# Performance work log

Measured on AMD Instinct MI355X. Metric: run time of the kernel, lower is better.

The kernel has to match this reference:

```python
import jax, jax.numpy as jnp
import numpy as np


def _gumbel_from_uniform(u):
    # u in (0,1) -> standard Gumbel noise
    u = jnp.clip(u, 1e-6, 1.0 - 1e-6)
    return -jnp.log(-jnp.log(u))


def _lsq(x, s, num_bits):
    # LSQ fake-quant: scale, clamp to signed range, round (STE), rescale.
    Qp = 2 ** (num_bits - 1) - 1
    Qn = -(2 ** (num_bits - 1))
    xs = x / s
    xc = jnp.clip(xs, Qn, Qp)
    xr = xc + jax.lax.stop_gradient(jnp.round(xc) - xc)
    return xr * s


def _hard_gumbel_softmax(logits, g, tau):
    y = jax.nn.softmax((logits + g) / tau, axis=-1)
    hard = jax.nn.one_hot(jnp.argmax(y, axis=-1), y.shape[-1], dtype=y.dtype)
    return hard + y - jax.lax.stop_gradient(y)


def setup_inputs() -> dict:
    key = jax.random.key(0)
    ks = jax.random.split(key, 16)
    B, L, K, N = 32, 1024, 64, 8
    v = jax.random.normal(ks[0], (B, L, K, 2), dtype=jnp.float32)
    H = jax.random.normal(ks[1], (B, L, N, K, 2), dtype=jnp.float32)
    local_snr = jax.random.uniform(ks[2], (B, L, K, 1), dtype=jnp.float32)
    g_demod = _gumbel_from_uniform(jax.random.uniform(ks[3], (B, L, K, 3), dtype=jnp.float32))
    g_channel = _gumbel_from_uniform(jax.random.uniform(ks[4], (B, L, K, 3), dtype=jnp.float32))
    # policy MLP params (in,out layout), kaiming-ish init
    W1 = jax.random.normal(ks[5], (5, 32), dtype=jnp.float32) * (2.0 / 5) ** 0.5
    b1 = jnp.zeros((32,), dtype=jnp.float32)
    W2 = jax.random.normal(ks[6], (32, 32), dtype=jnp.float32) * (2.0 / 32) ** 0.5
    b2 = jnp.zeros((32,), dtype=jnp.float32)
    Wd = jax.random.normal(ks[7], (32, 3), dtype=jnp.float32) * (1.0 / 32) ** 0.5
    bd = jnp.zeros((3,), dtype=jnp.float32)
    Wc = jax.random.normal(ks[8], (32, 3), dtype=jnp.float32) * (1.0 / 32) ** 0.5
    bc = jnp.zeros((3,), dtype=jnp.float32)
    # LSQ step sizes (scalars) matching init_s of the torch module
    s2d = jnp.float32(0.5)
    s4d = jnp.float32(0.1)
    s2c = jnp.float32(0.5)
    s4c = jnp.float32(0.1)
    return dict(v=v, H=H, local_snr=local_snr, g_demod=g_demod, g_channel=g_channel,
                W1=W1, b1=b1, W2=W2, b2=b2, Wd=Wd, bd=bd, Wc=Wc, bc=bc,
                s2d=s2d, s4d=s4d, s2c=s2c, s4c=s4c)


def reference(v, H, local_snr, g_demod, g_channel,
              W1, b1, W2, b2, Wd, bd, Wc, bc, s2d, s4d, s2c, s4c):
    tau = 1.0
    B, L, K, _ = v.shape
    N = H.shape[2]
    # channel power features: sum over antennas and re/im -> (B,L,K)
    h_power = jnp.sum(H * H, axis=(2, 4))
    channel_norm = h_power[..., None]                      # (B,L,K,1)
    avg_power = jnp.broadcast_to(jnp.mean(h_power, axis=1, keepdims=True), (B, L, K))[..., None]
    pin = jnp.concatenate([v[..., 0:1], v[..., 1:2], local_snr, channel_norm, avg_power], axis=-1)  # (B,L,K,5)
    # tiny router MLP
    h = jax.nn.relu(pin @ W1 + b1)
    h = jax.nn.relu(h @ W2 + b2)
    logits_demod = h @ Wd + bd                              # (B,L,K,3)
    logits_channel = h @ Wc + bc
    w_demod = _hard_gumbel_softmax(logits_demod, g_demod, tau)
    w_channel = _hard_gumbel_softmax(logits_channel, g_channel, tau)
    # weighted combine of fake-quantized branches (0-bit branch contributes 0)
    v_q = w_demod[..., 1:2] * _lsq(v, s2d, 2) + w_demod[..., 2:3] * _lsq(v, s4d, 4)
    w_ch = w_channel[:, :, None]                            # (B,L,1,K,3) broadcast over antennas
    H_q = w_ch[..., 1:2] * _lsq(H, s2c, 2) + w_ch[..., 2:3] * _lsq(H, s4c, 4)
    expected_bits_demod = w_demod[..., 1] * 4.0 + w_demod[..., 2] * 8.0
    expected_bits_channel = w_channel[..., 1] * (2.0 * N * 2) + w_channel[..., 2] * (2.0 * N * 4)
    return (v_q, H_q, expected_bits_demod, expected_bits_channel, w_demod, w_channel)
```

## Files before the change

kernel.cpp:

```cpp
#include <hip/hip_runtime.h>

namespace {
constexpr int Bb = 32, Ll = 1024, Kk = 64, Nn = 8;
constexpr int BLK = Bb * Ll * Kk;
constexpr long long HFLOATS = (long long)BLK * Nn * 2;
constexpr int CH = 16;
constexpr int LCH = Ll / CH;

constexpr long long OFF_VQ  = 0;
constexpr long long OFF_HQ  = (long long)BLK * 2;
constexpr long long OFF_EBD = OFF_HQ + HFLOATS;
constexpr long long OFF_EBC = OFF_EBD + BLK;
constexpr long long OFF_WD  = OFF_EBC + BLK;
constexpr long long OFF_WC  = OFF_WD + (long long)BLK*3;
}

__device__ __forceinline__ float lsq_i(float x, float inv, float s, float Qn, float Qp) {
    float xc = fminf(fmaxf(x * inv, Qn), Qp);
    return rintf(xc) * s;
}

__device__ __forceinline__ void hard_gumbel(float z0, float z1, float z2, float w[3]) {
    int arg = 0; float m = z0;
    if (z1 > m) { m = z1; arg = 1; }
    if (z2 > m) { m = z2; arg = 2; }
    float e0 = expf(z0 - m), e1 = expf(z1 - m), e2 = expf(z2 - m);
    float s  = e0 + e1 + e2;
    float y0 = e0 / s, y1 = e1 / s, y2 = e2 / s;
    w[0] = ((arg == 0 ? 1.0f : 0.0f) + y0) - y0;
    w[1] = ((arg == 1 ? 1.0f : 0.0f) + y1) - y1;
    w[2] = ((arg == 2 ? 1.0f : 0.0f) + y2) - y2;
}

__global__ __launch_bounds__(256) void hpa_kernel(const float* __restrict__ H,
                                                  double* __restrict__ partial) {
    int blk = blockIdx.x;
    int b   = blk >> 4;
    int c   = blk & (CH - 1);
    int t   = threadIdx.x;
    int k   = t & 63, ls = t >> 6;
    const float2* Hf = (const float2*)H;
    double acc = 0.0;
    int l0 = c * LCH + ls;
    for (int i = 0; i < LCH / 4; ++i) {
        int l = l0 + i * 4;
        const float2* Hb = Hf + (long long)(b * Ll + l) * (Nn * Kk) + k;
        double e = 0.0;
        #pragma unroll
        for (int n = 0; n < Nn; ++n) {
            float2 h = Hb[n * Kk];
            e += (double)(h.x * h.x);
            e += (double)(h.y * h.y);
        }
        acc += (double)(float)e;
    }
    __shared__ double sh[256];
    sh[t] = acc;
    __syncthreads();
    if (t < 64)
        partial[(long long)blk * 64 + t] =
            (sh[t] + sh[t + 64]) + (sh[t + 128] + sh[t + 192]);
}

__global__ __launch_bounds__(256) void fused_kernel(
    const float* __restrict__ v,  const float* __restrict__ snr,
    const float* __restrict__ gd, const float* __restrict__ gc,
    const float* __restrict__ W1, const float* __restrict__ b1,
    const float* __restrict__ W2, const float* __restrict__ b2,
    const float* __restrict__ Wd, const float* __restrict__ bd,
    const float* __restrict__ Wc, const float* __restrict__ bc,
    const float* __restrict__ ps2d, const float* __restrict__ ps4d,
    const float* __restrict__ ps2c, const float* __restrict__ ps4c,
    const double* __restrict__ partial,
    const float* __restrict__ H,
    float* __restrict__ out) {
    int idx = blockIdx.x * 256 + threadIdx.x;
    int b   = idx >> 16;
    int k   = idx & 63;
    int bl  = idx >> 6;

    const float2* Hf = (const float2*)H + (long long)bl * (Nn * Kk) + k;
    float2 hreg[Nn];
    #pragma unroll
    for (int n = 0; n < Nn; ++n) hreg[n] = Hf[n * Kk];

    double hacc = 0.0;
    #pragma unroll
    for (int n = 0; n < Nn; ++n) {
        hacc += (double)(hreg[n].x * hreg[n].x);
        hacc += (double)(hreg[n].y * hreg[n].y);
    }
    float p3 = (float)hacc;

    const double* pb = partial + (long long)b * (CH * 64) + k;
    double s = 0.0;
    #pragma unroll
    for (int c = 0; c < CH; ++c) s += pb[c * 64];
    float p4 = (float)(s * (1.0 / 1024.0));

    float2 vv = ((const float2*)v)[idx];
    float p0 = vv.x, p1 = vv.y;
    float p2 = snr[idx];

    float h1[32];
    #pragma unroll
    for (int i = 0; i < 32; ++i) {
        float a = b1[i];
        a = fmaf(p0, W1[i],       a);
        a = fmaf(p1, W1[32 + i],  a);
        a = fmaf(p2, W1[64 + i],  a);
        a = fmaf(p3, W1[96 + i],  a);
        a = fmaf(p4, W1[128 + i], a);
        h1[i] = fmaxf(a, 0.0f);
    }
    float h2[32];
    #pragma unroll
    for (int i = 0; i < 32; ++i) h2[i] = b2[i];
    #pragma unroll
    for (int j = 0; j < 32; ++j) {
        float hj = h1[j];
        #pragma unroll
        for (int i = 0; i < 32; ++i) h2[i] = fmaf(hj, W2[j * 32 + i], h2[i]);
    }
    #pragma unroll
    for (int i = 0; i < 32; ++i) h2[i] = fmaxf(h2[i], 0.0f);
    float ld[3] = { bd[0], bd[1], bd[2] };
    float lc[3] = { bc[0], bc[1], bc[2] };
    #pragma unroll
    for (int j = 0; j < 32; ++j) {
        float hj = h2[j];
        ld[0] = fmaf(hj, Wd[j * 3 + 0], ld[0]);
        ld[1] = fmaf(hj, Wd[j * 3 + 1], ld[1]);
        ld[2] = fmaf(hj, Wd[j * 3 + 2], ld[2]);
        lc[0] = fmaf(hj, Wc[j * 3 + 0], lc[0]);
        lc[1] = fmaf(hj, Wc[j * 3 + 1], lc[1]);
        lc[2] = fmaf(hj, Wc[j * 3 + 2], lc[2]);
    }

    long long i3 = (long long)idx * 3;
    float wdm[3], wch[3];
    hard_gumbel(ld[0] + gd[i3], ld[1] + gd[i3 + 1], ld[2] + gd[i3 + 2], wdm);
    hard_gumbel(lc[0] + gc[i3], lc[1] + gc[i3 + 1], lc[2] + gc[i3 + 2], wch);

    float s2d = *ps2d, s4d = *ps4d, s2c = *ps2c, s4c = *ps4c;
    float i2d = 1.0f / s2d, i4d = 1.0f / s4d, i2c = 1.0f / s2c, i4c = 1.0f / s4c;

    float q0 = wdm[1] * lsq_i(p0, i2d, s2d, -2.0f, 1.0f)
             + wdm[2] * lsq_i(p0, i4d, s4d, -8.0f, 7.0f);
    float q1 = wdm[1] * lsq_i(p1, i2d, s2d, -2.0f, 1.0f)
             + wdm[2] * lsq_i(p1, i4d, s4d, -8.0f, 7.0f);
    ((float2*)(out + OFF_VQ))[idx] = make_float2(q0, q1);

    out[OFF_EBD + idx] = wdm[1] * 4.0f + wdm[2] * 8.0f;
    out[OFF_EBC + idx] = wch[1] * 32.0f + wch[2] * 64.0f;
    out[OFF_WD + i3 + 0] = wdm[0];
    out[OFF_WD + i3 + 1] = wdm[1];
    out[OFF_WD + i3 + 2] = wdm[2];
    out[OFF_WC + i3 + 0] = wch[0];
    out[OFF_WC + i3 + 1] = wch[1];
    out[OFF_WC + i3 + 2] = wch[2];

    float w1c = wch[1], w2c = wch[2];
    float2* outHQ = (float2*)(out + OFF_HQ) + (long long)bl * (Nn * Kk) + k;
    #pragma unroll
    for (int n = 0; n < Nn; ++n) {
        float hx = hreg[n].x, hy = hreg[n].y;
        float qx = w1c * lsq_i(hx, i2c, s2c, -2.0f, 1.0f)
                 + w2c * lsq_i(hx, i4c, s4c, -8.0f, 7.0f);
        float qy = w1c * lsq_i(hy, i2c, s2c, -2.0f, 1.0f)
                 + w2c * lsq_i(hy, i4c, s4c, -8.0f, 7.0f);
        outHQ[n * Kk] = make_float2(qx, qy);
    }
}

extern "C" void kernel_launch(void* const* d_in, const int* in_sizes, int n_in,
                              void* d_out, int out_size, void* d_ws, size_t ws_size,
                              hipStream_t stream) {
    const float* v    = (const float*)d_in[0];
    const float* H    = (const float*)d_in[1];
    const float* snr  = (const float*)d_in[2];
    const float* gd   = (const float*)d_in[3];
    const float* gc   = (const float*)d_in[4];
    const float* W1   = (const float*)d_in[5];
    const float* b1   = (const float*)d_in[6];
    const float* W2   = (const float*)d_in[7];
    const float* b2   = (const float*)d_in[8];
    const float* Wd   = (const float*)d_in[9];
    const float* bd   = (const float*)d_in[10];
    const float* Wc   = (const float*)d_in[11];
    const float* bc   = (const float*)d_in[12];
    const float* s2d  = (const float*)d_in[13];
    const float* s4d  = (const float*)d_in[14];
    const float* s2c  = (const float*)d_in[15];
    const float* s4c  = (const float*)d_in[16];

    float* out = (float*)d_out;
    double* partial = (double*)d_ws;

    hpa_kernel<<<Bb * CH, 256, 0, stream>>>(H, partial);
    fused_kernel<<<BLK / 256, 256, 0, stream>>>(v, snr, gd, gc, W1, b1, W2, b2,
                                                Wd, bd, Wc, bc, s2d, s4d, s2c, s4c,
                                                partial, H, out);
}
```

Measured before the change: 436.7 us.

## Process two antennas per thread with float4 loads and stores

Each thread in both kernels now handles two adjacent k elements, using float4 loads of H and v plus wider stores for all outputs. The MLP weights are loaded once and applied to both elements, which halves the redundant weight reads per element. The softmax uses fast exp and one reciprocal instead of three divides. The H-power reduction is re-indexed to match the new layout. Register pressure roughly doubles with two 32-wide hidden vectors per thread, which may lower occupancy; the fused kernel also reads H twice instead of keeping it in registers.

After: 461.4 us. 1.06x slower.

```diff
diff --git a/kernel.cpp b/kernel.cpp
--- a/kernel.cpp
+++ b/kernel.cpp
@@ -24,9 +24,9 @@
     int arg = 0; float m = z0;
     if (z1 > m) { m = z1; arg = 1; }
     if (z2 > m) { m = z2; arg = 2; }
-    float e0 = expf(z0 - m), e1 = expf(z1 - m), e2 = expf(z2 - m);
-    float s  = e0 + e1 + e2;
-    float y0 = e0 / s, y1 = e1 / s, y2 = e2 / s;
+    float e0 = __expf(z0 - m), e1 = __expf(z1 - m), e2 = __expf(z2 - m);
+    float r  = 1.0f / (e0 + e1 + e2);
+    float y0 = e0 * r, y1 = e1 * r, y2 = e2 * r;
     w[0] = ((arg == 0 ? 1.0f : 0.0f) + y0) - y0;
     w[1] = ((arg == 1 ? 1.0f : 0.0f) + y1) - y1;
     w[2] = ((arg == 2 ? 1.0f : 0.0f) + y2) - y2;
@@ -38,28 +38,37 @@
     int b   = blk >> 4;
     int c   = blk & (CH - 1);
     int t   = threadIdx.x;
-    int k   = t & 63, ls = t >> 6;
-    const float2* Hf = (const float2*)H;
-    double acc = 0.0;
+    int kp  = t & 31;
+    int ls  = t >> 5;
+    const float4* Hf = (const float4*)H;
+    double acc0 = 0.0, acc1 = 0.0;
     int l0 = c * LCH + ls;
-    for (int i = 0; i < LCH / 4; ++i) {
-        int l = l0 + i * 4;
-        const float2* Hb = Hf + (long long)(b * Ll + l) * (Nn * Kk) + k;
-        double e = 0.0;
+    for (int i = 0; i < LCH / 8; ++i) {
+        int l = l0 + i * 8;
+        const float4* Hb = Hf + (long long)(b * Ll + l) * (Nn * 32) + kp;
+        double e0 = 0.0, e1 = 0.0;
         #pragma unroll
         for (int n = 0; n < Nn; ++n) {
-            float2 h = Hb[n * Kk];
-            e += (double)(h.x * h.x);
-            e += (double)(h.y * h.y);
+            float4 h = Hb[n * 32];
+            e0 += (double)(h.x * h.x);
+            e0 += (double)(h.y * h.y);
+            e1 += (double)(h.z * h.z);
+            e1 += (double)(h.w * h.w);
         }
-        acc += (double)(float)e;
-    }
-    __shared__ double sh[256];
-    sh[t] = acc;
+        acc0 += (double)(float)e0;
+        acc1 += (double)(float)e1;
+    }
+    __shared__ double sh[2][256];
+    sh[0][t] = acc0;
+    sh[1][t] = acc1;
     __syncthreads();
-    if (t < 64)
-        partial[(long long)blk * 64 + t] =
-            (sh[t] + sh[t + 64]) + (sh[t + 128] + sh[t + 192]);
+    if (t < 64) {
+        int kp2 = t & 31, sel = t >> 5;
+        double s = 0.0;
+        #pragma unroll
+        for (int l2 = 0; l2 < 8; ++l2) s += sh[sel][l2 * 32 + kp2];
+        partial[(long long)blk * 64 + 2 * kp2 + sel] = s;
+    }
 }
 
 __global__ __launch_bounds__(256) void fused_kernel(
@@ -74,102 +83,123 @@
     const double* __restrict__ partial,
     const float* __restrict__ H,
     float* __restrict__ out) {
-    int idx = blockIdx.x * 256 + threadIdx.x;
-    int b   = idx >> 16;
-    int k   = idx & 63;
-    int bl  = idx >> 6;
-
-    const float2* Hf = (const float2*)H + (long long)bl * (Nn * Kk) + k;
-    float2 hreg[Nn];
-    #pragma unroll
-    for (int n = 0; n < Nn; ++n) hreg[n] = Hf[n * Kk];
-
-    double hacc = 0.0;
+    int t  = blockIdx.x * 256 + threadIdx.x;
+    int b  = t >> 15;
+    int kp = t & 31;
+    int bl = t >> 5;
+
+    const float4* Hf = (const float4*)H + (long long)bl * (Nn * 32) + kp;
+    double e0 = 0.0, e1 = 0.0;
     #pragma unroll
     for (int n = 0; n < Nn; ++n) {
-        hacc += (double)(hreg[n].x * hreg[n].x);
-        hacc += (double)(hreg[n].y * hreg[n].y);
-    }
-    float p3 = (float)hacc;
-
-    const double* pb = partial + (long long)b * (CH * 64) + k;
-    double s = 0.0;
-    #pragma unroll
-    for (int c = 0; c < CH; ++c) s += pb[c * 64];
-    float p4 = (float)(s * (1.0 / 1024.0));
-
-    float2 vv = ((const float2*)v)[idx];
-    float p0 = vv.x, p1 = vv.y;
-    float p2 = snr[idx];
-
-    float h1[32];
+        float4 h = Hf[n * 32];
+        e0 += (double)(h.x * h.x);
+        e0 += (double)(h.y * h.y);
+        e1 += (double)(h.z * h.z);
+        e1 += (double)(h.w * h.w);
+    }
+    float p3a = (float)e0, p3b = (float)e1;
+
+    const double2* pb = (const double2*)(partial + (long long)b * (CH * 64)) + kp;
+    double s0 = 0.0, s1 = 0.0;
+    #pragma unroll
+    for (int c = 0; c < CH; ++c) { double2 p = pb[c * 32]; s0 += p.x; s1 += p.y; }
+    float p4a = (float)(s0 * (1.0 / 1024.0));
+    float p4b = (float)(s1 * (1.0 / 1024.0));
+
+    float4 vv = ((const float4*)v)[t];
+    float2 sn = ((const float2*)snr)[t];
+    float p0a = vv.x, p1a = vv.y, p2a = sn.x;
+    float p0b = vv.z, p1b = vv.w, p2b = sn.y;
+
+    const float2* gdp = (const float2*)gd + (long long)t * 3;
+    const float2* gcp = (const float2*)gc + (long long)t * 3;
+    float2 gd0 = gdp[0], gd1 = gdp[1], gd2 = gdp[2];
+    float2 gc0 = gcp[0], gc1 = gcp[1], gc2 = gcp[2];
+
+    float2 h1[32];
     #pragma unroll
     for (int i = 0; i < 32; ++i) {
-        float a = b1[i];
-        a = fmaf(p0, W1[i],       a);
-        a = fmaf(p1, W1[32 + i],  a);
-        a = fmaf(p2, W1[64 + i],  a);
-        a = fmaf(p3, W1[96 + i],  a);
-        a = fmaf(p4, W1[128 + i], a);
-        h1[i] = fmaxf(a, 0.0f);
-    }
-    float h2[32];
-    #pragma unroll
-    for (int i = 0; i < 32; ++i) h2[i] = b2[i];
+        float w0 = W1[i], w1 = W1[32+i], w2 = W1[64+i], w3 = W1[96+i], w4 = W1[128+i];
+        float aa = b1[i], ab = b1[i];
+        aa = fmaf(p0a, w0, aa);  ab = fmaf(p0b, w0, ab);
+        aa = fmaf(p1a, w1, aa);  ab = fmaf(p1b, w1, ab);
+        aa = fmaf(p2a, w2, aa);  ab = fmaf(p2b, w2, ab);
+        aa = fmaf(p3a, w3, aa);  ab = fmaf(p3b, w3, ab);
+        aa = fmaf(p4a, w4, aa);  ab = fmaf(p4b, w4, ab);
+        h1[i].x = fmaxf(aa, 0.0f);
+        h1[i].y = fmaxf(ab, 0.0f);
+    }
+    float2 h2[32];
+    #pragma unroll
+    for (int i = 0; i < 32; ++i) { h2[i].x = b2[i]; h2[i].y = b2[i]; }
     #pragma unroll
     for (int j = 0; j < 32; ++j) {
-        float hj = h1[j];
+        float2 hj = h1[j];
         #pragma unroll
-        for (int i = 0; i < 32; ++i) h2[i] = fmaf(hj, W2[j * 32 + i], h2[i]);
-    }
-    #pragma unroll
-    for (int i = 0; i < 32; ++i) h2[i] = fmaxf(h2[i], 0.0f);
-    float ld[3] = { bd[0], bd[1], bd[2] };
-    float lc[3] = { bc[0], bc[1], bc[2] };
+        for (int i = 0; i < 32; ++i) {
+            float w = W2[j * 32 + i];
+            h2[i].x = fmaf(hj.x, w, h2[i].x);
+            h2[i].y = fmaf(hj.y, w, h2[i].y);
+        }
+    }
+    #pragma unroll
+    for (int i = 0; i < 32; ++i) { h2[i].x = fmaxf(h2[i].x, 0.0f); h2[i].y = fmaxf(h2[i].y, 0.0f); }
+    float2 ld0 = {bd[0], bd[0]}, ld1 = {bd[1], bd[1]}, ld2 = {bd[2], bd[2]};
+    float2 lc0 = {bc[0], bc[0]}, lc1 = {bc[1], bc[1]}, lc2 = {bc[2], bc[2]};
     #pragma unroll
     for (int j = 0; j < 32; ++j) {
-        float hj = h2[j];
-        ld[0] = fmaf(hj, Wd[j * 3 + 0], ld[0]);
-        ld[1] = fmaf(hj, Wd[j * 3 + 1], ld[1]);
-        ld[2] = fmaf(hj, Wd[j * 3 + 2], ld[2]);
-        lc[0] = fmaf(hj, Wc[j * 3 + 0], lc[0]);
-        lc[1] = fmaf(hj, Wc[j * 3 + 1], lc[1]);
-        lc[2] = fmaf(hj, Wc[j * 3 + 2], lc[2]);
-    }
-
-    long long i3 = (long long)idx * 3;
-    float wdm[3], wch[3];
-    hard_gumbel(ld[0] + gd[i3], ld[1] + gd[i3 + 1], ld[2] + gd[i3 + 2], wdm);
-    hard_gumbel(lc[0] + gc[i3], lc[1] + gc[i3 + 1], lc[2] + gc[i3 + 2], wch);
+        float2 hj = h2[j];
+        float wd0 = Wd[j*3+0], wd1 = Wd[j*3+1], wd2 = Wd[j*3+2];
+        float wc0 = Wc[j*3+0], wc1 = Wc[j*3+1], wc2 = Wc[j*3+2];
+        ld0.x = fmaf(hj.x, wd0, ld0.x);  ld0.y = fmaf(hj.y, wd0, ld0.y);
+        ld1.x = fmaf(hj.x, wd1, ld1.x);  ld1.y = fmaf(hj.y, wd1, ld1.y);
+        ld2.x = fmaf(hj.x, wd2, ld2.x);  ld2.y = fmaf(hj.y, wd2, ld2.y);
+        lc0.x = fmaf(hj.x, wc0, lc0.x);  lc0.y = fmaf(hj.y, wc0, lc0.y);
+        lc1.x = fmaf(hj.x, wc1, lc1.x);  lc1.y = fmaf(hj.y, wc1, lc1.y);
+        lc2.x = fmaf(hj.x, wc2, lc2.x);  lc2.y = fmaf(hj.y, wc2, lc2.y);
+    }
+
+    float wdA[3], wdB[3], wcA[3], wcB[3];
+    hard_gumbel(ld0.x + gd0.x, ld1.x + gd0.y, ld2.x + gd1.x, wdA);
+    hard_gumbel(ld0.y + gd1.y, ld1.y + gd2.x, ld2.y + gd2.y, wdB);
+    hard_gumbel(lc0.x + gc0.x, lc1.x + gc0.y, lc2.x + gc1.x, wcA);
+    hard_gumbel(lc0.y + gc1.y, lc1.y + gc2.x, lc2.y + gc2.y, wcB);
 
     float s2d = *ps2d, s4d = *ps4d, s2c = *ps2c, s4c = *ps4c;
     float i2d = 1.0f / s2d, i4d = 1.0f / s4d, i2c = 1.0f / s2c, i4c = 1.0f / s4c;
 
-    float q0 = wdm[1] * lsq_i(p0, i2d, s2d, -2.0f, 1.0f)
-             + wdm[2] * lsq_i(p0, i4d, s4d, -8.0f, 7.0f);
-    float q1 = wdm[1] * lsq_i(p1, i2d, s2d, -2.0f, 1.0f)
-             + wdm[2] * lsq_i(p1, i4d, s4d, -8.0f, 7.0f);
-    ((float2*)(out + OFF_VQ))[idx] = make_float2(q0, q1);
-
-    out[OFF_EBD + idx] = wdm[1] * 4.0f + wdm[2] * 8.0f;
-    out[OFF_EBC + idx] = wch[1] * 32.0f + wch[2] * 64.0f;
-    out[OFF_WD + i3 + 0] = wdm[0];
-    out[OFF_WD + i3 + 1] = wdm[1];
-    out[OFF_WD + i3 + 2] = wdm[2];
-    out[OFF_WC + i3 + 0] = wch[0];
-    out[OFF_WC + i3 + 1] = wch[1];
-    out[OFF_WC + i3 + 2] = wch[2];
-
-    float w1c = wch[1], w2c = wch[2];
-    float2* outHQ = (float2*)(out + OFF_HQ) + (long long)bl * (Nn * Kk) + k;
+    float4 q;
+    q.x = wdA[1] * lsq_i(p0a, i2d, s2d, -2.0f, 1.0f) + wdA[2] * lsq_i(p0a, i4d, s4d, -8.0f, 7.0f);
+    q.y = wdA[1] * lsq_i(p1a, i2d, s2d, -2.0f, 1.0f) + wdA[2] * lsq_i(p1a, i4d, s4d, -8.0f, 7.0f);
+    q.z = wdB[1] * lsq_i(p0b, i2d, s2d, -2.0f, 1.0f) + wdB[2] * lsq_i(p0b, i4d, s4d, -8.0f, 7.0f);
+    q.w = wdB[1] * lsq_i(p1b, i2d, s2d, -2.0f, 1.0f) + wdB[2] * lsq_i(p1b, i4d, s4d, -8.0f, 7.0f);
+    ((float4*)(out + OFF_VQ))[t] = q;
+
+    ((float2*)(out + OFF_EBD))[t] = make_float2(wdA[1] * 4.0f + wdA[2] * 8.0f,
+                                                wdB[1] * 4.0f + wdB[2] * 8.0f);
+    ((float2*)(out + OFF_EBC))[t] = make_float2(wcA[1] * 32.0f + wcA[2] * 64.0f,
+                                                wcB[1] * 32.0f + wcB[2] * 64.0f);
+    float2* wdp = (float2*)(out + OFF_WD) + (long long)t * 3;
+    wdp[0] = make_float2(wdA[0], wdA[1]);
+    wdp[1] = make_float2(wdA[2], wdB[0]);
+    wdp[2] = make_float2(wdB[1], wdB[2]);
+    float2* wcp = (float2*)(out + OFF_WC) + (long long)t * 3;
+    wcp[0] = make_float2(wcA[0], wcA[1]);
+    wcp[1] = make_float2(wcA[2], wcB[0]);
+    wcp[2] = make_float2(wcB[1], wcB[2]);
+
+    float w1a = wcA[1], w2a = wcA[2], w1b = wcB[1], w2b = wcB[2];
+    float4* oq = (float4*)(out + OFF_HQ) + (long long)bl * (Nn * 32) + kp;
     #pragma unroll
     for (int n = 0; n < Nn; ++n) {
-        float hx = hreg[n].x, hy = hreg[n].y;
-        float qx = w1c * lsq_i(hx, i2c, s2c, -2.0f, 1.0f)
-                 + w2c * lsq_i(hx, i4c, s4c, -8.0f, 7.0f);
-        float qy = w1c * lsq_i(hy, i2c, s2c, -2.0f, 1.0f)
-                 + w2c * lsq_i(hy, i4c, s4c, -8.0f, 7.0f);
-        outHQ[n * Kk] = make_float2(qx, qy);
+        float4 h = Hf[n * 32];
+        float4 o;
+        o.x = w1a * lsq_i(h.x, i2c, s2c, -2.0f, 1.0f) + w2a * lsq_i(h.x, i4c, s4c, -8.0f, 7.0f);
+        o.y = w1a * lsq_i(h.y, i2c, s2c, -2.0f, 1.0f) + w2a * lsq_i(h.y, i4c, s4c, -8.0f, 7.0f);
+        o.z = w1b * lsq_i(h.z, i2c, s2c, -2.0f, 1.0f) + w2b * lsq_i(h.z, i4c, s4c, -8.0f, 7.0f);
+        o.w = w1b * lsq_i(h.w, i2c, s2c, -2.0f, 1.0f) + w2b * lsq_i(h.w, i4c, s4c, -8.0f, 7.0f);
+        oq[n * 32] = o;
     }
 }
 
@@ -198,7 +228,7 @@
     double* partial = (double*)d_ws;
 
     hpa_kernel<<<Bb * CH, 256, 0, stream>>>(H, partial);
-    fused_kernel<<<BLK / 256, 256, 0, stream>>>(v, snr, gd, gc, W1, b1, W2, b2,
-                                                Wd, bd, Wc, bc, s2d, s4d, s2c, s4c,
-                                                partial, H, out);
-}
+    fused_kernel<<<BLK / 2 / 256, 256, 0, stream>>>(v, snr, gd, gc, W1, b1, W2, b2,
+                                                    Wd, bd, Wc, bc, s2d, s4d, s2c, s4c,
+                                                    partial, H, out);
+}
```

## Cut register pressure in fused kernel, share avg power via LDS, widen H loads

Applied to the files above, without the earlier changes.

Several changes aimed at occupancy and memory efficiency. The fused kernel no longer holds H in registers across the MLP; it reloads H for the quantize pass. It also fuses layer 1 into the layer 2 loop so h1 need not be kept live, and requests 8 blocks per CU through launch_bounds. Per-batch average power is now computed once per block into shared memory rather than per thread. The power-reduction kernel reads float4, and the softmax uses fast exp and a reciprocal. The risks are a second read of H (which may hit in cache), spills if the launch_bounds cap is too tight, and small numeric differences from __expf.

New measurement: 522.3 us. 19.6% more time.

```diff
diff --git a/kernel.cpp b/kernel.cpp
--- a/kernel.cpp
+++ b/kernel.cpp
@@ -24,9 +24,9 @@
     int arg = 0; float m = z0;
     if (z1 > m) { m = z1; arg = 1; }
     if (z2 > m) { m = z2; arg = 2; }
-    float e0 = expf(z0 - m), e1 = expf(z1 - m), e2 = expf(z2 - m);
-    float s  = e0 + e1 + e2;
-    float y0 = e0 / s, y1 = e1 / s, y2 = e2 / s;
+    float e0 = __expf(z0 - m), e1 = __expf(z1 - m), e2 = __expf(z2 - m);
+    float r  = 1.0f / (e0 + e1 + e2);
+    float y0 = e0 * r, y1 = e1 * r, y2 = e2 * r;
     w[0] = ((arg == 0 ? 1.0f : 0.0f) + y0) - y0;
     w[1] = ((arg == 1 ? 1.0f : 0.0f) + y1) - y1;
     w[2] = ((arg == 2 ? 1.0f : 0.0f) + y2) - y2;
@@ -38,31 +38,40 @@
     int b   = blk >> 4;
     int c   = blk & (CH - 1);
     int t   = threadIdx.x;
-    int k   = t & 63, ls = t >> 6;
-    const float2* Hf = (const float2*)H;
-    double acc = 0.0;
+    int kp  = t & 31;
+    int ls  = t >> 5;
+    const float4* Hf = (const float4*)H;
+    double acc0 = 0.0, acc1 = 0.0;
     int l0 = c * LCH + ls;
-    for (int i = 0; i < LCH / 4; ++i) {
-        int l = l0 + i * 4;
-        const float2* Hb = Hf + (long long)(b * Ll + l) * (Nn * Kk) + k;
-        double e = 0.0;
+    for (int i = 0; i < LCH / 8; ++i) {
+        int l = l0 + i * 8;
+        const float4* Hb = Hf + (long long)(b * Ll + l) * (Nn * 32) + kp;
+        double e0 = 0.0, e1 = 0.0;
         #pragma unroll
         for (int n = 0; n < Nn; ++n) {
-            float2 h = Hb[n * Kk];
-            e += (double)(h.x * h.x);
-            e += (double)(h.y * h.y);
+            float4 h = Hb[n * 32];
+            e0 += (double)(h.x * h.x);
+            e0 += (double)(h.y * h.y);
+            e1 += (double)(h.z * h.z);
+            e1 += (double)(h.w * h.w);
         }
-        acc += (double)(float)e;
-    }
-    __shared__ double sh[256];
-    sh[t] = acc;
+        acc0 += (double)(float)e0;
+        acc1 += (double)(float)e1;
+    }
+    __shared__ double sh[2][256];
+    sh[0][t] = acc0;
+    sh[1][t] = acc1;
     __syncthreads();
-    if (t < 64)
-        partial[(long long)blk * 64 + t] =
-            (sh[t] + sh[t + 64]) + (sh[t + 128] + sh[t + 192]);
-}
-
-__global__ __launch_bounds__(256) void fused_kernel(
+    if (t < 64) {
+        int kp2 = t & 31, sel = t >> 5;
+        double s = 0.0;
+        #pragma unroll
+        for (int l2 = 0; l2 < 8; ++l2) s += sh[sel][l2 * 32 + kp2];
+        partial[(long long)blk * 64 + 2 * kp2 + sel] = s;
+    }
+}
+
+__global__ __launch_bounds__(256, 8) void fused_kernel(
     const float* __restrict__ v,  const float* __restrict__ snr,
     const float* __restrict__ gd, const float* __restrict__ gc,
     const float* __restrict__ W1, const float* __restrict__ b1,
@@ -75,72 +84,69 @@
     const float* __restrict__ H,
     float* __restrict__ out) {
     int idx = blockIdx.x * 256 + threadIdx.x;
+    int t   = threadIdx.x;
     int b   = idx >> 16;
     int k   = idx & 63;
     int bl  = idx >> 6;
 
+    __shared__ float avg_sh[64];
+    if (t < 64) {
+        const double* pb = partial + (long long)b * (CH * 64) + t;
+        double s = 0.0;
+        #pragma unroll
+        for (int c = 0; c < CH; ++c) s += pb[c * 64];
+        avg_sh[t] = (float)(s * (1.0 / 1024.0));
+    }
+
     const float2* Hf = (const float2*)H + (long long)bl * (Nn * Kk) + k;
-    float2 hreg[Nn];
-    #pragma unroll
-    for (int n = 0; n < Nn; ++n) hreg[n] = Hf[n * Kk];
-
     double hacc = 0.0;
     #pragma unroll
     for (int n = 0; n < Nn; ++n) {
-        hacc += (double)(hreg[n].x * hreg[n].x);
-        hacc += (double)(hreg[n].y * hreg[n].y);
+        float2 h = Hf[n * Kk];
+        hacc += (double)(h.x * h.x);
+        hacc += (double)(h.y * h.y);
     }
     float p3 = (float)hacc;
 
-    const double* pb = partial + (long long)b * (CH * 64) + k;
-    double s = 0.0;
-    #pragma unroll
-    for (int c = 0; c < CH; ++c) s += pb[c * 64];
-    float p4 = (float)(s * (1.0 / 1024.0));
+    __syncthreads();
+    float p4 = avg_sh[k];
 
     float2 vv = ((const float2*)v)[idx];
     float p0 = vv.x, p1 = vv.y;
     float p2 = snr[idx];
 
-    float h1[32];
-    #pragma unroll
-    for (int i = 0; i < 32; ++i) {
-        float a = b1[i];
-        a = fmaf(p0, W1[i],       a);
-        a = fmaf(p1, W1[32 + i],  a);
-        a = fmaf(p2, W1[64 + i],  a);
-        a = fmaf(p3, W1[96 + i],  a);
-        a = fmaf(p4, W1[128 + i], a);
-        h1[i] = fmaxf(a, 0.0f);
-    }
     float h2[32];
     #pragma unroll
     for (int i = 0; i < 32; ++i) h2[i] = b2[i];
     #pragma unroll
     for (int j = 0; j < 32; ++j) {
-        float hj = h1[j];
+        float a = b1[j];
+        a = fmaf(p0, W1[j],       a);
+        a = fmaf(p1, W1[32 + j],  a);
+        a = fmaf(p2, W1[64 + j],  a);
+        a = fmaf(p3, W1[96 + j],  a);
+        a = fmaf(p4, W1[128 + j], a);
+        float hj = fmaxf(a, 0.0f);
         #pragma unroll
         for (int i = 0; i < 32; ++i) h2[i] = fmaf(hj, W2[j * 32 + i], h2[i]);
     }
-    #pragma unroll
-    for (int i = 0; i < 32; ++i) h2[i] = fmaxf(h2[i], 0.0f);
-    float ld[3] = { bd[0], bd[1], bd[2] };
-    float lc[3] = { bc[0], bc[1], bc[2] };
+    float ld0 = bd[0], ld1 = bd[1], ld2 = bd[2];
+    float lc0 = bc[0], lc1 = bc[1], lc2 = bc[2];
     #pragma unroll
     for (int j = 0; j < 32; ++j) {
-        float hj = h2[j];
-        ld[0] = fmaf(hj, Wd[j * 3 + 0], ld[0]);
-        ld[1] = fmaf(hj, Wd[j * 3 + 1], ld[1]);
-        ld[2] = fmaf(hj, Wd[j * 3 + 2], ld[2]);
-        lc[0] = fmaf(hj, Wc[j * 3 + 0], lc[0]);
-        lc[1] = fmaf(hj, Wc[j * 3 + 1], lc[1]);
-        lc[2] = fmaf(hj, Wc[j * 3 + 2], lc[2]);
+        float hj = fmaxf(h2[j], 0.0f);
+        ld0 = fmaf(hj, Wd[j * 3 + 0], ld0);
+        ld1 = fmaf(hj, Wd[j * 3 + 1], ld1);
+        ld2 = fmaf(hj, Wd[j * 3 + 2], ld2);
+        lc0 = fmaf(hj, Wc[j * 3 + 0], lc0);
+        lc1 = fmaf(hj, Wc[j * 3 + 1], lc1);
+        lc2 = fmaf(hj, Wc[j * 3 + 2], lc2);
     }
 
     long long i3 = (long long)idx * 3;
     float wdm[3], wch[3];
-    hard_gumbel(ld[0] + gd[i3], ld[1] + gd[i3 + 1], ld[2] + gd[i3 + 2], wdm);
-    hard_gumbel(lc[0] + gc[i3], lc[1] + gc[i3 + 1], lc[2] + gc[i3 + 2], wch);
+    hard_gumbel(ld0 + gd[i3], ld1 + gd[i3 + 1], ld2 + gd[i3 + 2], wdm);
+    hard_gumbel(lc0 + gc[i3], lc1 + gc[i3 + 1], lc2 + gc[i3 + 2], wch);
 
     float s2d = *ps2d, s4d = *ps4d, s2c = *ps2c, s4c = *ps4c;
     float i2d = 1.0f / s2d, i4d = 1.0f / s4d, i2c = 1.0f / s2c, i4c = 1.0f / s4c;
@@ -164,11 +170,11 @@
     float2* outHQ = (float2*)(out + OFF_HQ) + (long long)bl * (Nn * Kk) + k;
     #pragma unroll
     for (int n = 0; n < Nn; ++n) {
-        float hx = hreg[n].x, hy = hreg[n].y;
-        float qx = w1c * lsq_i(hx, i2c, s2c, -2.0f, 1.0f)
-                 + w2c * lsq_i(hx, i4c, s4c, -8.0f, 7.0f);
-        float qy = w1c * lsq_i(hy, i2c, s2c, -2.0f, 1.0f)
-                 + w2c * lsq_i(hy, i4c, s4c, -8.0f, 7.0f);
+        float2 h = Hf[n * Kk];
+        float qx = w1c * lsq_i(h.x, i2c, s2c, -2.0f, 1.0f)
+                 + w2c * lsq_i(h.x, i4c, s4c, -8.0f, 7.0f);
+        float qy = w1c * lsq_i(h.y, i2c, s2c, -2.0f, 1.0f)
+                 + w2c * lsq_i(h.y, i4c, s4c, -8.0f, 7.0f);
         outHQ[n * Kk] = make_float2(qx, qy);
     }
 }
```
